# Kernel tuning notes

Measured on AMD Instinct MI355X. Metric: run time of the kernel, lower is better.

## Reference

```python
import jax, jax.numpy as jnp
import numpy as np

N = 50000      # nodes
E = 600000     # edges
C = 128        # in_channels
H = 128        # hidden_channels
O = 128        # out_channels
G = 512        # graphs in batch
BN_EPS = 1e-5


def setup_inputs() -> dict:
    key = jax.random.key(0)
    ks = jax.random.split(key, 16)

    def w(k, shape):
        return jax.random.normal(k, shape, dtype=jnp.float32) * 0.05

    inp = {}
    inp["x"] = jax.random.normal(ks[0], (N, C), dtype=jnp.float32)
    inp["edge_index"] = jax.random.randint(ks[1], (2, E), 0, N, dtype=jnp.int64)
    inp["batch"] = jnp.sort(jax.random.randint(ks[2], (N,), 0, G, dtype=jnp.int64))

    dims = [(C, H, H), (H, H, H), (H, H, O)]
    ki = 3
    for li, (din, dh, dout) in enumerate(dims, 1):
        inp[f"g{li}_W1"] = w(ks[ki], (din, dh)); inp[f"g{li}_b1"] = jnp.zeros((dh,), jnp.float32)
        inp[f"g{li}_gm"] = jnp.ones((dh,), jnp.float32); inp[f"g{li}_bt"] = jnp.zeros((dh,), jnp.float32)
        inp[f"g{li}_rm"] = jnp.zeros((dh,), jnp.float32); inp[f"g{li}_rv"] = jnp.ones((dh,), jnp.float32)
        inp[f"g{li}_W2"] = w(ks[ki + 1], (dh, dout)); inp[f"g{li}_b2"] = jnp.zeros((dout,), jnp.float32)
        ki += 2
    inp["lin_W"] = w(ks[ki], (H + H + O, O))
    inp["lin_b"] = jnp.zeros((O,), jnp.float32)
    return inp


def gin_conv(x, src, dst, W1, b1, gm, bt, rm, rv, W2, b2):
    # GINConv (eps=0): mlp(x + sum_{j in N(i)} x_j); mlp = Linear-BN(eval)-ReLU-Linear
    agg = jax.ops.segment_sum(x[src], dst, num_segments=N)   # [N, d] scatter-add
    h = (x + agg) @ W1 + b1
    h = (h - rm) * jax.lax.rsqrt(rv + BN_EPS) * gm + bt      # BatchNorm1d, eval mode
    return jax.nn.relu(h) @ W2 + b2


def reference(x, edge_index, batch,
              g1_W1, g1_b1, g1_gm, g1_bt, g1_rm, g1_rv, g1_W2, g1_b2,
              g2_W1, g2_b1, g2_gm, g2_bt, g2_rm, g2_rv, g2_W2, g2_b2,
              g3_W1, g3_b1, g3_gm, g3_bt, g3_rm, g3_rv, g3_W2, g3_b2,
              lin_W, lin_b):
    src, dst = edge_index[0], edge_index[1]
    # dropout(0.2) is identity in eval mode
    x1 = jax.nn.relu(gin_conv(x, src, dst, g1_W1, g1_b1, g1_gm, g1_bt, g1_rm, g1_rv, g1_W2, g1_b2))
    x2 = jax.nn.relu(gin_conv(x1, src, dst, g2_W1, g2_b1, g2_gm, g2_bt, g2_rm, g2_rv, g2_W2, g2_b2))
    x3 = gin_conv(x2, src, dst, g3_W1, g3_b1, g3_gm, g3_bt, g3_rm, g3_rv, g3_W2, g3_b2)
    xc = jnp.concatenate([x1, x2, x3], axis=-1)              # JumpingKnowledge 'cat' -> [N, H+H+O]
    sums = jax.ops.segment_sum(xc, batch, num_segments=G)    # global_mean_pool
    cnt = jax.ops.segment_sum(jnp.ones((N, 1), xc.dtype), batch, num_segments=G)
    pooled = sums / jnp.maximum(cnt, 1.0)                    # [G, H+H+O]
    return pooled @ lin_W + lin_b                            # [G, O]
```

## Files before the change

kernel.cpp:

```cpp
#include <hip/hip_runtime.h>
#include <hip/hip_bf16.h>

#define NNODES 50000
#define NEDGES 600000
#define NGRAPHS 512
#define BN_EPS 1e-5f

typedef short bf16x8 __attribute__((ext_vector_type(8)));
typedef float f32x4 __attribute__((ext_vector_type(4)));

__device__ __forceinline__ void bf_split(float x, ushort& h, ushort& l) {
    __hip_bfloat16 bh = __float2bfloat16(x);
    float r = x - __bfloat162float(bh);
    __hip_bfloat16 bl = __float2bfloat16(r);
    h = __builtin_bit_cast(ushort, bh);
    l = __builtin_bit_cast(ushort, bl);
}
__device__ __forceinline__ ushort f2b(float x) {
    return __builtin_bit_cast(ushort, __float2bfloat16(x));
}
__device__ __forceinline__ float b2f(ushort u) {
    union { uint i; float f; } c; c.i = ((uint)u) << 16; return c.f;
}
__device__ __forceinline__ float blo(uint u) {
    union { uint i; float f; } c; c.i = u << 16; return c.f;
}
__device__ __forceinline__ float bhi(uint u) {
    union { uint i; float f; } c; c.i = u & 0xffff0000u; return c.f;
}

__global__ __launch_bounds__(256) void prep_kernel(
    const float* __restrict__ x, ushort* __restrict__ xh,
    float* __restrict__ pooled, const int* __restrict__ dst,
    int* __restrict__ counts, int* __restrict__ row_ptr,
    const float* W0, const float* W1, const float* W2, const float* W3,
    const float* W4, const float* W5, ushort* __restrict__ hi, ushort* __restrict__ lo) {
    int b = blockIdx.x, t = threadIdx.x;
    if (b < 3125) {
        int f4 = b * 512 + t * 2;
        float4 a0 = ((const float4*)x)[f4];
        float4 a1 = ((const float4*)x)[f4 + 1];
        ushort4 u0 = {f2b(a0.x), f2b(a0.y), f2b(a0.z), f2b(a0.w)};
        ushort4 u1 = {f2b(a1.x), f2b(a1.y), f2b(a1.z), f2b(a1.w)};
        int e0 = f4 * 4;
        *(ushort4*)(xh + e0) = u0;
        *(ushort4*)(xh + e0 + 4) = u1;
        if (b == 0 && t == 0) row_ptr[NNODES] = NEDGES;
    } else if (b < 3317) {
        ((float4*)pooled)[(b - 3125) * 256 + t] = make_float4(0.f, 0.f, 0.f, 0.f);
    } else if (b < 5661) {
        int i = (b - 3317) * 256 + t;
        if (i < NEDGES) atomicAdd(&counts[dst[i]], 1);
    } else {
        int wb = b - 5661;
        const float* Ws[6] = {W0, W1, W2, W3, W4, W5};
        const float* W = Ws[wb >> 4];
        ushort* h = hi + (size_t)(wb >> 4) * 16384;
        ushort* l = lo + (size_t)(wb >> 4) * 16384;
        int chunk = wb & 15;
#pragma unroll
        for (int i = 0; i < 4; i++) {
            int idx = chunk * 1024 + i * 256 + t;
            int j    = idx & 7;
            int lane = (idx >> 3) & 63;
            int nt   = (idx >> 9) & 7;
            int kb   = (idx >> 12) & 3;
            int k = kb * 32 + ((lane >> 4) << 3) + j;
            int n = nt * 16 + (lane & 15);
            ushort hh, ll;
            bf_split(W[k * 128 + n], hh, ll);
            h[idx] = hh;
            l[idx] = ll;
        }
    }
}

__global__ __launch_bounds__(256) void scan1_kernel(const int* __restrict__ counts,
                                                    int* __restrict__ partials, int n) {
    __shared__ int s[256];
    int i = blockIdx.x * 256 + threadIdx.x;
    int v = (i < n) ? counts[i] : 0;
    s[threadIdx.x] = v;
    __syncthreads();
    for (int off = 128; off > 0; off >>= 1) {
        if (threadIdx.x < off) s[threadIdx.x] += s[threadIdx.x + off];
        __syncthreads();
    }
    if (threadIdx.x == 0) partials[blockIdx.x] = s[0];
}

__global__ __launch_bounds__(256) void scan3_kernel(const int* __restrict__ counts,
                                                    const int* __restrict__ partials,
                                                    int* __restrict__ row_ptr,
                                                    int* __restrict__ cursor, int n, int nb) {
    __shared__ int s[256];
    __shared__ int base_sh;
    int t = threadIdx.x;
    int pv = (t < (int)blockIdx.x && t < nb) ? partials[t] : 0;
    s[t] = pv;
    __syncthreads();
    for (int off = 128; off > 0; off >>= 1) {
        if (t < off) s[t] += s[t + off];
        __syncthreads();
    }
    if (t == 0) base_sh = s[0];
    __syncthreads();
    int base = base_sh;
    int i = blockIdx.x * 256 + t;
    int v = (i < n) ? counts[i] : 0;
    __syncthreads();
    s[t] = v;
    __syncthreads();
    for (int off = 1; off < 256; off <<= 1) {
        int nv = (t >= off) ? s[t - off] : 0;
        __syncthreads();
        s[t] += nv;
        __syncthreads();
    }
    if (i < n) {
        int ex = base + s[t] - v;
        row_ptr[i] = ex;
        cursor[i] = ex;
    }
}

__global__ __launch_bounds__(256) void scatter_kernel(const int* __restrict__ src,
                                                      const int* __restrict__ dst,
                                                      int* __restrict__ cursor,
                                                      int* __restrict__ esrc, int E) {
    int i = blockIdx.x * 256 + threadIdx.x;
    if (i < E) {
        int p = atomicAdd(&cursor[dst[i]], 1);
        esrc[p] = src[i];
    }
}

__global__ __launch_bounds__(256) void agg_kernel(
    const ushort* __restrict__ phi,
    const int* __restrict__ rp, const int* __restrict__ esrc,
    ushort* __restrict__ ohi, int n) {
    int wid  = (blockIdx.x * 256 + threadIdx.x) >> 6;
    int lane = threadIdx.x & 63;
    int node = wid * 4 + (lane >> 4);
    int q = lane & 15;
    if (node >= n) return;
    const uint4* xv = (const uint4*)phi;
    uint4 s0 = xv[(size_t)node * 16 + q];
    float acc[8];
    acc[0] = blo(s0.x); acc[1] = bhi(s0.x);
    acc[2] = blo(s0.y); acc[3] = bhi(s0.y);
    acc[4] = blo(s0.z); acc[5] = bhi(s0.z);
    acc[6] = blo(s0.w); acc[7] = bhi(s0.w);
    int e = rp[node], end = rp[node + 1];
    for (; e + 8 <= end; e += 8) {
        int i0 = esrc[e],     i1 = esrc[e + 1], i2 = esrc[e + 2], i3 = esrc[e + 3];
        int i4 = esrc[e + 4], i5 = esrc[e + 5], i6 = esrc[e + 6], i7 = esrc[e + 7];
        uint4 v0 = xv[(size_t)i0 * 16 + q];
        uint4 v1 = xv[(size_t)i1 * 16 + q];
        uint4 v2 = xv[(size_t)i2 * 16 + q];
        uint4 v3 = xv[(size_t)i3 * 16 + q];
        uint4 v4 = xv[(size_t)i4 * 16 + q];
        uint4 v5 = xv[(size_t)i5 * 16 + q];
        uint4 v6 = xv[(size_t)i6 * 16 + q];
        uint4 v7 = xv[(size_t)i7 * 16 + q];
        acc[0] += ((blo(v0.x) + blo(v1.x)) + (blo(v2.x) + blo(v3.x))) +
                  ((blo(v4.x) + blo(v5.x)) + (blo(v6.x) + blo(v7.x)));
        acc[1] += ((bhi(v0.x) + bhi(v1.x)) + (bhi(v2.x) + bhi(v3.x))) +
                  ((bhi(v4.x) + bhi(v5.x)) + (bhi(v6.x) + bhi(v7.x)));
        acc[2] += ((blo(v0.y) + blo(v1.y)) + (blo(v2.y) + blo(v3.y))) +
                  ((blo(v4.y) + blo(v5.y)) + (blo(v6.y) + blo(v7.y)));
        acc[3] += ((bhi(v0.y) + bhi(v1.y)) + (bhi(v2.y) + bhi(v3.y))) +
                  ((bhi(v4.y) + bhi(v5.y)) + (bhi(v6.y) + bhi(v7.y)));
        acc[4] += ((blo(v0.z) + blo(v1.z)) + (blo(v2.z) + blo(v3.z))) +
                  ((blo(v4.z) + blo(v5.z)) + (blo(v6.z) + blo(v7.z)));
        acc[5] += ((bhi(v0.z) + bhi(v1.z)) + (bhi(v2.z) + bhi(v3.z))) +
                  ((bhi(v4.z) + bhi(v5.z)) + (bhi(v6.z) + bhi(v7.z)));
        acc[6] += ((blo(v0.w) + blo(v1.w)) + (blo(v2.w) + blo(v3.w))) +
                  ((blo(v4.w) + blo(v5.w)) + (blo(v6.w) + blo(v7.w)));
        acc[7] += ((bhi(v0.w) + bhi(v1.w)) + (bhi(v2.w) + bhi(v3.w))) +
                  ((bhi(v4.w) + bhi(v5.w)) + (bhi(v6.w) + bhi(v7.w)));
    }
    for (; e + 2 <= end; e += 2) {
        int i0 = esrc[e], i1 = esrc[e + 1];
        uint4 v0 = xv[(size_t)i0 * 16 + q];
        uint4 v1 = xv[(size_t)i1 * 16 + q];
        acc[0] += blo(v0.x) + blo(v1.x); acc[1] += bhi(v0.x) + bhi(v1.x);
        acc[2] += blo(v0.y) + blo(v1.y); acc[3] += bhi(v0.y) + bhi(v1.y);
        acc[4] += blo(v0.z) + blo(v1.z); acc[5] += bhi(v0.z) + bhi(v1.z);
        acc[6] += blo(v0.w) + blo(v1.w); acc[7] += bhi(v0.w) + bhi(v1.w);
    }
    for (; e < end; e++) {
        uint4 v = xv[(size_t)esrc[e] * 16 + q];
        acc[0] += blo(v.x); acc[1] += bhi(v.x);
        acc[2] += blo(v.y); acc[3] += bhi(v.y);
        acc[4] += blo(v.z); acc[5] += bhi(v.z);
        acc[6] += blo(v.w); acc[7] += bhi(v.w);
    }
    uint4 o;
    o.x = (uint)f2b(acc[0]) | ((uint)f2b(acc[1]) << 16);
    o.y = (uint)f2b(acc[2]) | ((uint)f2b(acc[3]) << 16);
    o.z = (uint)f2b(acc[4]) | ((uint)f2b(acc[5]) << 16);
    o.w = (uint)f2b(acc[6]) | ((uint)f2b(acc[7]) << 16);
    *(uint4*)(ohi + (size_t)node * 128 + q * 8) = o;
}

template <bool RELU_OUT, bool WRITE_PLANES>
__global__ __launch_bounds__(128) void mlp_kernel(
    const ushort* __restrict__ Ah,
    const ushort* __restrict__ W1hi, const ushort* __restrict__ W1lo,
    const ushort* __restrict__ W2hi, const ushort* __restrict__ W2lo,
    const float* __restrict__ b1, const float* __restrict__ gm,
    const float* __restrict__ bt, const float* __restrict__ rm,
    const float* __restrict__ rv, const float* __restrict__ b2,
    ushort* __restrict__ Ch,
    const int* __restrict__ batch, float* __restrict__ pooled, int poff, int M) {
    __shared__ __align__(16) ushort smem[64 * 136];
    __shared__ int bsm[64];
    const int t = threadIdx.x;
    const int lane = t & 63;
    const int wv = t >> 6;
    const int row0 = blockIdx.x * 64;
    const int g = lane >> 4, c = lane & 15;

    if (t < 64) bsm[t] = (row0 + t < M) ? batch[row0 + t] : -1;

    const int m0 = t >> 2, k80 = (t & 3) * 8;
    const int m1 = m0 + 32;
    int r0 = row0 + m0; if (r0 >= M) r0 = M - 1;
    int r1 = row0 + m1; if (r1 >= M) r1 = M - 1;
    const size_t ga0 = (size_t)r0 * 128 + k80;
    const size_t ga1 = (size_t)r1 * 128 + k80;
    const int la0 = m0 * 32 + k80, la1 = m1 * 32 + k80;

    f32x4 acc[4][4];
#pragma unroll
    for (int i = 0; i < 4; i++)
#pragma unroll
        for (int j = 0; j < 4; j++) acc[i][j] = (f32x4){0.f, 0.f, 0.f, 0.f};

    uint4 ph0 = *(const uint4*)(Ah + ga0);
    uint4 ph1 = *(const uint4*)(Ah + ga1);
    *(uint4*)&smem[la0] = ph0;
    *(uint4*)&smem[la1] = ph1;
    __syncthreads();

    int cur = 0;
    for (int kb = 0; kb < 4; kb++) {
        bf16x8 bh[4], bl[4];
#pragma unroll
        for (int ct = 0; ct < 4; ct++) {
            const size_t wo = (((size_t)kb * 8 + (wv * 4 + ct)) * 64 + lane) * 8;
            bh[ct] = *(const bf16x8*)(W1hi + wo);
            bl[ct] = *(const bf16x8*)(W1lo + wo);
        }
        if (kb < 3) {
            const size_t o = (size_t)(kb + 1) * 32;
            ph0 = *(const uint4*)(Ah + ga0 + o);
            ph1 = *(const uint4*)(Ah + ga1 + o);
        }
        bf16x8 ah[4];
#pragma unroll
        for (int rt = 0; rt < 4; rt++) {
            int off = cur * 4096 + (rt * 16 + c) * 32 + g * 8;
            ah[rt] = *(bf16x8*)&smem[off];
        }
#pragma unroll
        for (int rt = 0; rt < 4; rt++)
#pragma unroll
            for (int ct = 0; ct < 4; ct++) {
                acc[rt][ct] = __builtin_amdgcn_mfma_f32_16x16x32_bf16(ah[rt], bh[ct], acc[rt][ct], 0, 0, 0);
                acc[rt][ct] = __builtin_amdgcn_mfma_f32_16x16x32_bf16(ah[rt], bl[ct], acc[rt][ct], 0, 0, 0);
            }
        if (kb < 3) {
            *(uint4*)&smem[(cur ^ 1) * 4096 + la0] = ph0;
            *(uint4*)&smem[(cur ^ 1) * 4096 + la1] = ph1;
        }
        __syncthreads();
        cur ^= 1;
    }

    {
        float cs[4], ca[4];
#pragma unroll
        for (int ct = 0; ct < 4; ct++) {
            int n = wv * 64 + ct * 16 + c;
            float s = gm[n] * rsqrtf(rv[n] + BN_EPS);
            cs[ct] = s;
            ca[ct] = (b1[n] - rm[n]) * s + bt[n];
        }
#pragma unroll
        for (int rt = 0; rt < 4; rt++)
#pragma unroll
            for (int r = 0; r < 4; r++) {
                int row = rt * 16 + g * 4 + r;
#pragma unroll
                for (int ct = 0; ct < 4; ct++) {
                    int col = wv * 64 + ct * 16 + c;
                    float v = fmaxf(acc[rt][ct][r] * cs[ct] + ca[ct], 0.f);
                    smem[row * 136 + col] = f2b(v);
                }
            }
    }
    __syncthreads();

#pragma unroll
    for (int i = 0; i < 4; i++)
#pragma unroll
        for (int j = 0; j < 4; j++) acc[i][j] = (f32x4){0.f, 0.f, 0.f, 0.f};

    for (int kb = 0; kb < 4; kb++) {
        bf16x8 bh[4], bl[4];
#pragma unroll
        for (int ct = 0; ct < 4; ct++) {
            const size_t wo = (((size_t)kb * 8 + (wv * 4 + ct)) * 64 + lane) * 8;
            bh[ct] = *(const bf16x8*)(W2hi + wo);
            bl[ct] = *(const bf16x8*)(W2lo + wo);
        }
        bf16x8 ah[4];
#pragma unroll
        for (int rt = 0; rt < 4; rt++) {
            int off = (rt * 16 + c) * 136 + kb * 32 + g * 8;
            ah[rt] = *(bf16x8*)&smem[off];
        }
#pragma unroll
        for (int rt = 0; rt < 4; rt++)
#pragma unroll
            for (int ct = 0; ct < 4; ct++) {
                acc[rt][ct] = __builtin_amdgcn_mfma_f32_16x16x32_bf16(ah[rt], bh[ct], acc[rt][ct], 0, 0, 0);
                acc[rt][ct] = __builtin_amdgcn_mfma_f32_16x16x32_bf16(ah[rt], bl[ct], acc[rt][ct], 0, 0, 0);
            }
    }
    __syncthreads();

    {
        float ca2[4];
#pragma unroll
        for (int ct = 0; ct < 4; ct++) ca2[ct] = b2[wv * 64 + ct * 16 + c];
#pragma unroll
        for (int rt = 0; rt < 4; rt++)
#pragma unroll
            for (int r = 0; r < 4; r++) {
                int rl = rt * 16 + g * 4 + r;
                int row = row0 + rl;
                bool valid = row < M;
#pragma unroll
                for (int ct = 0; ct < 4; ct++) {
                    int col = wv * 64 + ct * 16 + c;
                    float v = acc[rt][ct][r] + ca2[ct];
                    if (RELU_OUT) v = fmaxf(v, 0.f);
                    ushort hh = f2b(valid ? v : 0.f);
                    smem[rl * 136 + col] = hh;
                    if (WRITE_PLANES && valid) Ch[(size_t)row * 128 + col] = hh;
                }
            }
    }
    __syncthreads();

    {
        int col = t;
        int gcur = bsm[0];
        float accp = 0.f;
#pragma unroll 8
        for (int r = 0; r < 64; r++) {
            int gg = bsm[r];
            if (gg != gcur) {
                if (gcur >= 0) atomicAdd(&pooled[gcur * 384 + poff + col], accp);
                accp = 0.f;
                gcur = gg;
            }
            accp += b2f(smem[r * 136 + col]);
        }
        if (gcur >= 0) atomicAdd(&pooled[gcur * 384 + poff + col], accp);
    }
}

__global__ __launch_bounds__(128) void final_kernel(const float* __restrict__ pooled,
                                                    const int* __restrict__ batch,
                                                    const float* __restrict__ W,
                                                    const float* __restrict__ b,
                                                    float* __restrict__ out, int n) {
    __shared__ float ps[384];
    int gph = blockIdx.x, t = threadIdx.x;
    int lo1 = 0, hi1 = n;
    while (lo1 < hi1) { int mid = (lo1 + hi1) >> 1; if (batch[mid] < gph) lo1 = mid + 1; else hi1 = mid; }
    int start = lo1;
    int lo2 = start, hi2 = n;
    while (lo2 < hi2) { int mid = (lo2 + hi2) >> 1; if (batch[mid] < gph + 1) lo2 = mid + 1; else hi2 = mid; }
    int cnt = lo2 - start;
    float inv = 1.f / (float)(cnt > 0 ? cnt : 1);
    for (int i = t; i < 384; i += 128) ps[i] = pooled[gph * 384 + i] * inv;
    __syncthreads();
    float acc = b[t];
#pragma unroll 8
    for (int k = 0; k < 384; k++) acc += ps[k] * W[k * 128 + t];
    out[gph * 128 + t] = acc;
}

extern "C" void kernel_launch(void* const* d_in, const int* in_sizes, int n_in,
                              void* d_out, int out_size, void* d_ws, size_t ws_size,
                              hipStream_t stream) {
    const float* x     = (const float*)d_in[0];
    const int*   edge  = (const int*)d_in[1];
    const int*   batch = (const int*)d_in[2];
    const float* p[32];
    for (int i = 0; i < n_in && i < 32; i++) p[i] = (const float*)d_in[i];
    const float* lin_W = p[27];
    const float* lin_b = p[28];

    char* w = (char*)d_ws;
    auto alloc = [&](size_t bytes) { void* r = (void*)w; w += (bytes + 255) & ~(size_t)255; return r; };
    const size_t PL = (size_t)NNODES * 128;
    ushort* thi   = (ushort*)alloc(PL * 2);
    ushort* xh0   = (ushort*)alloc(PL * 2);
    ushort* p1h   = (ushort*)alloc(PL * 2);
    ushort* p2h   = xh0;
    float* pooled = (float*)alloc((size_t)NGRAPHS * 384 * 4);
    int* counts   = (int*)alloc((size_t)NNODES * 4);
    int* cursor   = (int*)alloc((size_t)NNODES * 4);
    int* row_ptr  = (int*)alloc((size_t)(NNODES + 1) * 4);
    int* esrc     = (int*)alloc((size_t)NEDGES * 4);
    int* partials = (int*)alloc(256 * 4);
    ushort* wt_hi = (ushort*)alloc((size_t)6 * 16384 * 2);
    ushort* wt_lo = (ushort*)alloc((size_t)6 * 16384 * 2);

    const int* src = edge;
    const int* dst = edge + NEDGES;

    hipMemsetAsync(counts, 0, (size_t)NNODES * 4, stream);
    prep_kernel<<<5757, 256, 0, stream>>>(x, xh0, pooled, dst, counts, row_ptr,
                                          p[3], p[9], p[11], p[17], p[19], p[25],
                                          wt_hi, wt_lo);

    int nb = (NNODES + 255) / 256;
    scan1_kernel<<<nb, 256, 0, stream>>>(counts, partials, NNODES);
    scan3_kernel<<<nb, 256, 0, stream>>>(counts, partials, row_ptr, cursor, NNODES, nb);
    scatter_kernel<<<(NEDGES + 255) / 256, 256, 0, stream>>>(src, dst, cursor, esrc, NEDGES);

    int mlp_grid = (NNODES + 63) / 64;
    int agg_grid = (NNODES / 4 * 64 + 255) / 256;

    agg_kernel<<<agg_grid, 256, 0, stream>>>(xh0, row_ptr, esrc, thi, NNODES);
    mlp_kernel<true, true><<<mlp_grid, 128, 0, stream>>>(thi,
        wt_hi + 0 * 16384, wt_lo + 0 * 16384, wt_hi + 1 * 16384, wt_lo + 1 * 16384,
        p[4], p[5], p[6], p[7], p[8], p[10], p1h, batch, pooled, 0, NNODES);
    agg_kernel<<<agg_grid, 256, 0, stream>>>(p1h, row_ptr, esrc, thi, NNODES);
    mlp_kernel<true, true><<<mlp_grid, 128, 0, stream>>>(thi,
        wt_hi + 2 * 16384, wt_lo + 2 * 16384, wt_hi + 3 * 16384, wt_lo + 3 * 16384,
        p[12], p[13], p[14], p[15], p[16], p[18], p2h, batch, pooled, 128, NNODES);
    agg_kernel<<<agg_grid, 256, 0, stream>>>(p2h, row_ptr, esrc, thi, NNODES);
    mlp_kernel<false, false><<<mlp_grid, 128, 0, stream>>>(thi,
        wt_hi + 4 * 16384, wt_lo + 4 * 16384, wt_hi + 5 * 16384, wt_lo + 5 * 16384,
        p[20], p[21], p[22], p[23], p[24], p[26], nullptr, batch, pooled, 256, NNODES);

    final_kernel<<<NGRAPHS, 128, 0, stream>>>(pooled, batch, lin_W, lin_b,
                                              (float*)d_out, NNODES);
}
```

Measured before the change: 341.2 us.

## Merge setup, scan and CSR scatter into one cooperative persistent kernel

Replaces the memset, prep, two scan kernels and the scatter kernel with a single cooperative launch of 1024 blocks that uses grid-wide syncs between phases. The aim is to remove several kernel launch gaps and the separate memset. In exchange, every phase now runs on a fixed grid with grid-stride loops and pays grid.sync barriers, which may leave the lightweight scan phases underused and adds cooperative-launch constraints.

```diff
diff --git a/kernel.cpp b/kernel.cpp
--- a/kernel.cpp
+++ b/kernel.cpp
@@ -1,5 +1,8 @@
 #include <hip/hip_runtime.h>
 #include <hip/hip_bf16.h>
+#include <hip/hip_cooperative_groups.h>
+
+namespace cg = cooperative_groups;
 
 #define NNODES 50000
 #define NEDGES 600000
@@ -29,15 +32,25 @@
     union { uint i; float f; } c; c.i = u & 0xffff0000u; return c.f;
 }
 
-__global__ __launch_bounds__(256) void prep_kernel(
+__global__ __launch_bounds__(256, 4) void setup_kernel(
     const float* __restrict__ x, ushort* __restrict__ xh,
-    float* __restrict__ pooled, const int* __restrict__ dst,
-    int* __restrict__ counts, int* __restrict__ row_ptr,
-    const float* W0, const float* W1, const float* W2, const float* W3,
-    const float* W4, const float* W5, ushort* __restrict__ hi, ushort* __restrict__ lo) {
-    int b = blockIdx.x, t = threadIdx.x;
-    if (b < 3125) {
-        int f4 = b * 512 + t * 2;
+    float* __restrict__ pooled,
+    const int* __restrict__ src, const int* __restrict__ dst,
+    int* __restrict__ counts, int* __restrict__ cursor,
+    int* __restrict__ row_ptr, int* __restrict__ esrc,
+    int* __restrict__ partials,
+    const float* W0, const float* W1, const float* W2,
+    const float* W3, const float* W4, const float* W5,
+    ushort* __restrict__ hi, ushort* __restrict__ lo) {
+    cg::grid_group grid = cg::this_grid();
+    const int t = threadIdx.x;
+    const int tid = blockIdx.x * 256 + t;
+    const int nth = gridDim.x * 256;
+
+    for (int i = tid; i < NNODES; i += nth) counts[i] = 0;
+    if (tid == 0) row_ptr[NNODES] = NEDGES;
+    for (int i = tid; i < 800000; i += nth) {
+        int f4 = i * 2;
         float4 a0 = ((const float4*)x)[f4];
         float4 a1 = ((const float4*)x)[f4 + 1];
         ushort4 u0 = {f2b(a0.x), f2b(a0.y), f2b(a0.z), f2b(a0.w)};
@@ -45,91 +58,73 @@
         int e0 = f4 * 4;
         *(ushort4*)(xh + e0) = u0;
         *(ushort4*)(xh + e0 + 4) = u1;
-        if (b == 0 && t == 0) row_ptr[NNODES] = NEDGES;
-    } else if (b < 3317) {
-        ((float4*)pooled)[(b - 3125) * 256 + t] = make_float4(0.f, 0.f, 0.f, 0.f);
-    } else if (b < 5661) {
-        int i = (b - 3317) * 256 + t;
-        if (i < NEDGES) atomicAdd(&counts[dst[i]], 1);
-    } else {
-        int wb = b - 5661;
+    }
+    for (int i = tid; i < NGRAPHS * 96; i += nth)
+        ((float4*)pooled)[i] = make_float4(0.f, 0.f, 0.f, 0.f);
+    {
         const float* Ws[6] = {W0, W1, W2, W3, W4, W5};
-        const float* W = Ws[wb >> 4];
-        ushort* h = hi + (size_t)(wb >> 4) * 16384;
-        ushort* l = lo + (size_t)(wb >> 4) * 16384;
-        int chunk = wb & 15;
-#pragma unroll
-        for (int i = 0; i < 4; i++) {
-            int idx = chunk * 1024 + i * 256 + t;
+        for (int i = tid; i < 6 * 16384; i += nth) {
+            int mat = i >> 14, idx = i & 16383;
             int j    = idx & 7;
             int lane = (idx >> 3) & 63;
-            int nt   = (idx >> 9) & 7;
+            int nt2  = (idx >> 9) & 7;
             int kb   = (idx >> 12) & 3;
             int k = kb * 32 + ((lane >> 4) << 3) + j;
-            int n = nt * 16 + (lane & 15);
+            int n = nt2 * 16 + (lane & 15);
             ushort hh, ll;
-            bf_split(W[k * 128 + n], hh, ll);
-            h[idx] = hh;
-            l[idx] = ll;
-        }
-    }
-}
-
-__global__ __launch_bounds__(256) void scan1_kernel(const int* __restrict__ counts,
-                                                    int* __restrict__ partials, int n) {
-    __shared__ int s[256];
-    int i = blockIdx.x * 256 + threadIdx.x;
-    int v = (i < n) ? counts[i] : 0;
-    s[threadIdx.x] = v;
-    __syncthreads();
-    for (int off = 128; off > 0; off >>= 1) {
-        if (threadIdx.x < off) s[threadIdx.x] += s[threadIdx.x + off];
-        __syncthreads();
-    }
-    if (threadIdx.x == 0) partials[blockIdx.x] = s[0];
-}
-
-__global__ __launch_bounds__(256) void scan3_kernel(const int* __restrict__ counts,
-                                                    const int* __restrict__ partials,
-                                                    int* __restrict__ row_ptr,
-                                                    int* __restrict__ cursor, int n, int nb) {
+            bf_split(Ws[mat][k * 128 + n], hh, ll);
+            hi[(size_t)mat * 16384 + idx] = hh;
+            lo[(size_t)mat * 16384 + idx] = ll;
+        }
+    }
+    grid.sync();
+    for (int i = tid; i < NEDGES; i += nth) atomicAdd(&counts[dst[i]], 1);
+    grid.sync();
     __shared__ int s[256];
     __shared__ int base_sh;
-    int t = threadIdx.x;
-    int pv = (t < (int)blockIdx.x && t < nb) ? partials[t] : 0;
-    s[t] = pv;
-    __syncthreads();
-    for (int off = 128; off > 0; off >>= 1) {
-        if (t < off) s[t] += s[t + off];
-        __syncthreads();
-    }
-    if (t == 0) base_sh = s[0];
-    __syncthreads();
-    int base = base_sh;
-    int i = blockIdx.x * 256 + t;
-    int v = (i < n) ? counts[i] : 0;
-    __syncthreads();
-    s[t] = v;
-    __syncthreads();
-    for (int off = 1; off < 256; off <<= 1) {
-        int nv = (t >= off) ? s[t - off] : 0;
-        __syncthreads();
-        s[t] += nv;
-        __syncthreads();
-    }
-    if (i < n) {
-        int ex = base + s[t] - v;
-        row_ptr[i] = ex;
-        cursor[i] = ex;
-    }
-}
-
-__global__ __launch_bounds__(256) void scatter_kernel(const int* __restrict__ src,
-                                                      const int* __restrict__ dst,
-                                                      int* __restrict__ cursor,
-                                                      int* __restrict__ esrc, int E) {
-    int i = blockIdx.x * 256 + threadIdx.x;
-    if (i < E) {
+    const int nb = (NNODES + 255) / 256;
+    if ((int)blockIdx.x < nb) {
+        int i = blockIdx.x * 256 + t;
+        int v = (i < NNODES) ? counts[i] : 0;
+        s[t] = v;
+        __syncthreads();
+        for (int off = 128; off > 0; off >>= 1) {
+            if (t < off) s[t] += s[t + off];
+            __syncthreads();
+        }
+        if (t == 0) partials[blockIdx.x] = s[0];
+    }
+    grid.sync();
+    if ((int)blockIdx.x < nb) {
+        int pv = (t < (int)blockIdx.x && t < nb) ? partials[t] : 0;
+        s[t] = pv;
+        __syncthreads();
+        for (int off = 128; off > 0; off >>= 1) {
+            if (t < off) s[t] += s[t + off];
+            __syncthreads();
+        }
+        if (t == 0) base_sh = s[0];
+        __syncthreads();
+        int base = base_sh;
+        int i = blockIdx.x * 256 + t;
+        int v = (i < NNODES) ? counts[i] : 0;
+        __syncthreads();
+        s[t] = v;
+        __syncthreads();
+        for (int off = 1; off < 256; off <<= 1) {
+            int nv = (t >= off) ? s[t - off] : 0;
+            __syncthreads();
+            s[t] += nv;
+            __syncthreads();
+        }
+        if (i < NNODES) {
+            int ex = base + s[t] - v;
+            row_ptr[i] = ex;
+            cursor[i] = ex;
+        }
+    }
+    grid.sync();
+    for (int i = tid; i < NEDGES; i += nth) {
         int p = atomicAdd(&cursor[dst[i]], 1);
         esrc[p] = src[i];
     }
@@ -426,15 +421,18 @@
     const int* src = edge;
     const int* dst = edge + NEDGES;
 
-    hipMemsetAsync(counts, 0, (size_t)NNODES * 4, stream);
-    prep_kernel<<<5757, 256, 0, stream>>>(x, xh0, pooled, dst, counts, row_ptr,
-                                          p[3], p[9], p[11], p[17], p[19], p[25],
-                                          wt_hi, wt_lo);
-
-    int nb = (NNODES + 255) / 256;
-    scan1_kernel<<<nb, 256, 0, stream>>>(counts, partials, NNODES);
-    scan3_kernel<<<nb, 256, 0, stream>>>(counts, partials, row_ptr, cursor, NNODES, nb);
-    scatter_kernel<<<(NEDGES + 255) / 256, 256, 0, stream>>>(src, dst, cursor, esrc, NEDGES);
+    {
+        const float* W0 = p[3], *W1 = p[9], *W2 = p[11], *W3 = p[17], *W4 = p[19], *W5 = p[25];
+        void* args[] = {(void*)&x, (void*)&xh0, (void*)&pooled,
+                        (void*)&src, (void*)&dst,
+                        (void*)&counts, (void*)&cursor, (void*)&row_ptr,
+                        (void*)&esrc, (void*)&partials,
+                        (void*)&W0, (void*)&W1, (void*)&W2,
+                        (void*)&W3, (void*)&W4, (void*)&W5,
+                        (void*)&wt_hi, (void*)&wt_lo};
+        hipLaunchCooperativeKernel((void*)setup_kernel, dim3(1024), dim3(256),
+                                   args, 0, stream);
+    }
 
     int mlp_grid = (NNODES + 63) / 64;
     int agg_grid = (NNODES / 4 * 64 + 255) / 256;
```

New measurement: 783.5 us. 130% more time.
